# Optimization experiments

Hardware: AMD Instinct MI355X
Metric: run time of the kernel (lower is better)

The kernel has to match this reference:

```python
import jax, jax.numpy as jnp
import numpy as np

B, S, D, H, DK = 4, 1024, 1024, 16, 64  # batch, seq (nq=nk=max_seq_len), d_model, heads, d_kqv
NEG = -1e9
BERN_P = 0.3


def setup_inputs() -> dict:
    key = jax.random.key(0)
    ks = jax.random.split(key, 12)
    xavier = lambda k, fi, fo: jax.random.uniform(k, (fi, fo), minval=-1.0, maxval=1.0) * np.sqrt(6.0 / (fi + fo))
    return {
        "x": jax.random.normal(ks[0], (B, S, D), dtype=jnp.float32),
        "mask": jax.random.randint(ks[1], (B, S), 0, 2).astype(bool),
        "pos_att": jax.random.normal(ks[2], (B, S, S), dtype=jnp.float32),
        "decoder_mask": 1,
        "Wq": xavier(ks[3], D, H * DK), "bq": jnp.zeros((H * DK,), jnp.float32),
        "Wk": xavier(ks[4], D, H * DK), "bk": jnp.zeros((H * DK,), jnp.float32),
        "Wv": xavier(ks[5], D, H * DK), "bv": jnp.zeros((H * DK,), jnp.float32),
        "Wo": xavier(ks[6], H * DK, D), "bo": jnp.zeros((D,), jnp.float32),
    }


def _forward(x, pos_att, Wq, bq, Wk, bk, Wv, bv, Wo, bo, mask, decoder_mask):
    b_s, nq, _ = x.shape
    nk = nq  # self-attention
    relu = jax.nn.relu
    # projections (Linear + activation), split into heads
    q = relu(x @ Wq + bq).reshape(b_s, nq, H, DK).transpose(0, 2, 1, 3)  # [b,h,q,d]
    k = relu(x @ Wk + bk).reshape(b_s, nk, H, DK).transpose(0, 2, 1, 3)  # [b,h,k,d]
    v = relu(x @ Wv + bv).reshape(b_s, nk, H, DK).transpose(0, 2, 1, 3)  # [b,h,k,d]
    att = jnp.einsum("bhqd,bhkd->bhqk", q, k) / np.sqrt(DK).astype(np.float32)
    # positional bias broadcast over heads
    att = att + pos_att[:, None, :, :]
    # bernoulli(0.3) noise: each kept score gets -1e9 added (deterministic key)
    bern = jax.random.bernoulli(jax.random.key(42), BERN_P, att.shape)
    att = att + bern.astype(att.dtype) * NEG
    # key-padding mask [b,1,1,nk]
    att = jnp.where(mask[:, None, None, :], NEG, att)
    # causal triu mask (decoder_mask=True path)
    if decoder_mask:
        tri = jnp.triu(jnp.ones((nq, nk), dtype=bool), k=1)
        att = jnp.where(tri[None, None, :, :], NEG, att)
    att = jax.nn.softmax(att, axis=-1)
    out = jnp.einsum("bhqk,bhkd->bqhd", att, v).reshape(b_s, nq, H * DK)
    out = relu(out @ Wo + bo)
    return out


def reference(x, mask, pos_att, decoder_mask, Wq, bq, Wk, bk, Wv, bv, Wo, bo):
    return _forward(x, pos_att, Wq, bq, Wk, bk, Wv, bv, Wo, bo, mask, decoder_mask)
```

## Files before the change

kernel.cpp:

```cpp
#include <hip/hip_runtime.h>
#include <hip/hip_bf16.h>

#define NEGV (-1e9f)

typedef __attribute__((ext_vector_type(4))) float f32x4;
typedef __attribute__((ext_vector_type(8))) short short8;

#define MFMA_BF16(a, b, c) __builtin_amdgcn_mfma_f32_16x16x32_bf16((a), (b), (c), 0, 0, 0)

#define GLOAD_LDS16(gsrc, ldst)                                                        \
    __builtin_amdgcn_global_load_lds(                                                  \
        (const __attribute__((address_space(1))) unsigned int*)(gsrc),                 \
        (__attribute__((address_space(3))) unsigned int*)(ldst), 16, 0, 0)

#define GLOAD_LDS4(gsrc, ldst)                                                         \
    __builtin_amdgcn_global_load_lds(                                                  \
        (const __attribute__((address_space(1))) unsigned int*)(gsrc),                 \
        (__attribute__((address_space(3))) unsigned int*)(ldst), 4, 0, 0)

__device__ __forceinline__ unsigned short f2bf(float f) {
    union { float f; unsigned u; } v; v.f = f;
    return (unsigned short)((v.u + 0x7fffu + ((v.u >> 16) & 1u)) >> 16);
}

__device__ __forceinline__ float bf2f(unsigned short u) {
    return __uint_as_float((unsigned)u << 16);
}

#define ROTL(x, r) __builtin_amdgcn_alignbit((x), (x), 32 - (r))

__device__ __forceinline__ unsigned tf_bits(unsigned idx) {
    const unsigned ks0 = 0u, ks1 = 42u, ks2 = 0x1BD11BDAu ^ 0u ^ 42u;
    unsigned x0 = ks0, x1 = idx + ks1;
#define TFR(r) { x0 += x1; x1 = ROTL(x1, (r)); x1 ^= x0; }
    TFR(13) TFR(15) TFR(26) TFR(6)   x0 += ks1; x1 += ks2 + 1u;
    TFR(17) TFR(29) TFR(16) TFR(24)  x0 += ks2; x1 += ks0 + 2u;
    TFR(13) TFR(15) TFR(26) TFR(6)   x0 += ks0; x1 += ks1 + 3u;
    TFR(17) TFR(29) TFR(16) TFR(24)  x0 += ks1; x1 += ks2 + 4u;
    TFR(13) TFR(15) TFR(26) TFR(6)   x0 += ks2; x1 += ks0 + 5u;
#undef TFR
    return x0 ^ x1;
}
#define BERN_THRESH 1288490496u

__global__ __launch_bounds__(256) void prep_bern_kernel(
    const float* __restrict__ x,
    const float* __restrict__ Wq, const float* __restrict__ Wk,
    const float* __restrict__ Wv, const float* __restrict__ Wo,
    const float* __restrict__ bq, const float* __restrict__ bk,
    const float* __restrict__ bv,
    const unsigned* __restrict__ mraw, const unsigned* __restrict__ dec,
    unsigned short* __restrict__ xb, unsigned short* __restrict__ wcat,
    unsigned short* __restrict__ wto, float* __restrict__ bcat,
    int* __restrict__ mcanon, unsigned long long* __restrict__ bw) {
    __shared__ float ts[64][68];
    __shared__ int fl_gt1, fl_nf, fl_odz;
    const int bid = blockIdx.x;
    const int t = threadIdx.x;

    if (bid & 1) {
        const int dm = (dec[0] != 0u) ? 1 : 0;
        const int wgid = ((bid >> 1) << 2) + (t >> 6);
        const int lane = t & 63;
        const int G = dm ? 139264 : 262144;
        for (int g = wgid; g < G; g += 6144) {
            int f = __builtin_amdgcn_readfirstlane(g) << 2;
            int kw;
            if (dm) {
                kw = 0;
                while (f >= ((16 - kw) << 12)) { f -= (16 - kw) << 12; ++kw; }
            } else {
                kw = f >> 16; f &= 65535;
            }
            const int qoff = f >> 6;
            const int bh0 = f & 63;
            const int q = (dm ? (kw << 6) : 0) + qoff;
            const unsigned base = ((unsigned)q << 10) + ((unsigned)kw << 6) + (unsigned)lane;
            const unsigned i0 = base + ((unsigned)(bh0 + 0) << 20);
            const unsigned i1 = base + ((unsigned)(bh0 + 1) << 20);
            const unsigned i2 = base + ((unsigned)(bh0 + 2) << 20);
            const unsigned i3 = base + ((unsigned)(bh0 + 3) << 20);
            const unsigned r0 = tf_bits(i0), r1 = tf_bits(i1);
            const unsigned r2 = tf_bits(i2), r3 = tf_bits(i3);
            const unsigned long long w0 = __ballot(r0 < BERN_THRESH);
            const unsigned long long w1 = __ballot(r1 < BERN_THRESH);
            const unsigned long long w2 = __ballot(r2 < BERN_THRESH);
            const unsigned long long w3 = __ballot(r3 < BERN_THRESH);
            if (lane == 0) {
                const size_t rb = ((size_t)(((bh0 << 10) + q) << 4)) + (size_t)kw;
                bw[rb]         = w0;
                bw[rb + 16384] = w1;
                bw[rb + 32768] = w2;
                bw[rb + 49152] = w3;
            }
        }
    } else {
        const int idx = bid >> 1;
        if (idx < 1024) {
            const int which = idx >> 8, tile = idx & 255;
            const float* W = (which == 0) ? Wq : (which == 1) ? Wk : (which == 2) ? Wv : Wo;
            unsigned short* WT = (which < 3) ? (wcat + (size_t)which * 1048576u) : wto;
            const int k0 = (tile >> 4) * 64, n0 = (tile & 15) * 64;
            const int r = t >> 4, c4 = (t & 15) * 4;
#pragma unroll
            for (int rr = 0; rr < 4; ++rr) {
                const int row = r + rr * 16;
                float4 v = *reinterpret_cast<const float4*>(&W[(size_t)(k0 + row) * 1024 + n0 + c4]);
                ts[row][c4 + 0] = v.x; ts[row][c4 + 1] = v.y;
                ts[row][c4 + 2] = v.z; ts[row][c4 + 3] = v.w;
            }
            __syncthreads();
#pragma unroll
            for (int rr = 0; rr < 4; ++rr) {
                const int n = r + rr * 16;
                ushort4 o;
                o.x = f2bf(ts[c4 + 0][n]); o.y = f2bf(ts[c4 + 1][n]);
                o.z = f2bf(ts[c4 + 2][n]); o.w = f2bf(ts[c4 + 3][n]);
                *reinterpret_cast<ushort4*>(&WT[(size_t)(n0 + n) * 1024 + k0 + c4]) = o;
            }
        } else if (idx < 1536) {
            const int c = idx - 1024;
            const float* src = x + (size_t)c * 8192;
            unsigned short* dst = xb + (size_t)c * 8192;
#pragma unroll
            for (int j = 0; j < 8; ++j) {
                const int off = j * 1024 + t * 4;
                float4 v = *reinterpret_cast<const float4*>(src + off);
                ushort4 o;
                o.x = f2bf(v.x); o.y = f2bf(v.y); o.z = f2bf(v.z); o.w = f2bf(v.w);
                *reinterpret_cast<ushort4*>(dst + off) = o;
            }
        } else {
            if (t == 0) { fl_gt1 = 0; fl_nf = 0; fl_odz = 0; }
            __syncthreads();
            for (int i = t; i < 1024; i += 256) {
                unsigned w0 = mraw[i];
                if (w0 > 1u) fl_gt1 = 1;
                if (w0 != 0u && w0 != 1u && w0 != 0x3f800000u) fl_nf = 1;
                if ((i & 1) && w0 != 0u) fl_odz = 1;
            }
            __syncthreads();
            int mode;
            if (!fl_gt1)      mode = fl_odz ? 0 : 3;
            else if (!fl_nf)  mode = 2;
            else              mode = 1;
            for (int i = t; i < 4096; i += 256) {
                int v;
                if (mode == 0)      v = (int)mraw[i];
                else if (mode == 1) v = ((const unsigned char*)mraw)[i] ? 1 : 0;
                else if (mode == 2) v = (mraw[i] != 0u) ? 1 : 0;
                else                v = (mraw[2 * i] != 0u) ? 1 : 0;
                mcanon[i] = v;
            }
            for (int i = t; i < 3072; i += 256)
                bcat[i] = (i < 1024) ? bq[i] : ((i < 2048) ? bk[i - 1024] : bv[i - 2048]);
        }
    }
}

template<int MF, int WMODE>
__global__ __launch_bounds__(256) void gemm_bf16(
    const unsigned short* __restrict__ A, const unsigned short* __restrict__ BT,
    const float* __restrict__ bias, void* __restrict__ Cout,
    int M, int N, int K) {
    __shared__ unsigned short As[MF * 2048];
    __shared__ unsigned short Bs[8192];
    const int t = threadIdx.x;
    const int lane = t & 63, w = t >> 6;
    const int wr = w >> 1, wc = w & 1;
    const int lgrp = lane >> 4, l15 = lane & 15;
    const int m0 = blockIdx.y * (MF * 32), n0 = blockIdx.x * 128;
    const int srow = t >> 3;
    const int scol = ((t & 7) ^ (srow & 7)) << 3;
    const int rdsw = (l15 & 7) << 4;
    f32x4 acc[MF][4] = {};

    for (int k0 = 0; k0 < K; k0 += 64) {
#pragma unroll
        for (int s = 0; s < MF; ++s)
            GLOAD_LDS16(&A[(size_t)(m0 + s * 32 + srow) * K + (k0 + scol)], &As[s * 2048 + t * 8]);
#pragma unroll
        for (int s = 0; s < 4; ++s)
            GLOAD_LDS16(&BT[(size_t)(n0 + s * 32 + srow) * K + (k0 + scol)], &Bs[s * 2048 + t * 8]);
        __syncthreads();
#pragma unroll
        for (int kkh = 0; kkh < 2; ++kkh) {
            const int klb = (kkh * 32 + (lgrp << 3)) * 2;
            short8 af[MF], bf[4];
#pragma unroll
            for (int i = 0; i < MF; ++i)
                af[i] = *(const short8*)((const char*)As + (wr * (MF * 16) + i * 16 + l15) * 128 + (klb ^ rdsw));
#pragma unroll
            for (int i = 0; i < 4; ++i)
                bf[i] = *(const short8*)((const char*)Bs + (wc * 64 + i * 16 + l15) * 128 + (klb ^ rdsw));
            __builtin_amdgcn_s_setprio(1);
#pragma unroll
            for (int mf = 0; mf < MF; ++mf)
#pragma unroll
                for (int nf = 0; nf < 4; ++nf)
                    acc[mf][nf] = MFMA_BF16(af[mf], bf[nf], acc[mf][nf]);
            __builtin_amdgcn_s_setprio(0);
        }
        __syncthreads();
    }
#pragma unroll
    for (int nf = 0; nf < 4; ++nf) {
        const int n = n0 + wc * 64 + nf * 16 + l15;
        const float bv = bias[n];
#pragma unroll
        for (int mf = 0; mf < MF; ++mf) {
#pragma unroll
            for (int r = 0; r < 4; ++r) {
                const int m = m0 + wr * (MF * 16) + mf * 16 + (lgrp << 2) + r;
                float v = fmaxf(acc[mf][nf][r] + bv, 0.f);
                if (WMODE == 0) {
                    ((float*)Cout)[(size_t)m * N + n] = v;
                } else if (WMODE == 1) {
                    ((unsigned short*)Cout)[(size_t)m * N + n] = f2bf(v);
                } else {
                    const int which = n >> 10;
                    ((unsigned short*)Cout)[(size_t)which * 4194304u + (size_t)m * 1024 + (n & 1023)] = f2bf(v);
                }
            }
        }
    }
}

__global__ __launch_bounds__(256) void vsum_part(const unsigned short* __restrict__ Vb,
                                                 float* __restrict__ part) {
    const int c = blockIdx.x, b = blockIdx.y, t = threadIdx.x;
    float a0 = 0, a1 = 0, a2 = 0, a3 = 0;
    const unsigned short* src = &Vb[((size_t)(b * 1024 + c * 64)) * 1024 + t * 4];
    for (int r = 0; r < 64; ++r) {
        ushort4 v = *(const ushort4*)(src + (size_t)r * 1024);
        a0 += bf2f(v.x); a1 += bf2f(v.y); a2 += bf2f(v.z); a3 += bf2f(v.w);
    }
    float4 o = {a0, a1, a2, a3};
    *(float4*)&part[(size_t)(b * 16 + c) * 1024 + t * 4] = o;
}

__global__ __launch_bounds__(256) void vsum_reduce(const float* __restrict__ part,
                                                   float* __restrict__ vmean) {
    const int b = blockIdx.x, t = threadIdx.x;
    float4 s = {0, 0, 0, 0};
    for (int c = 0; c < 16; ++c) {
        float4 v = *(const float4*)&part[(size_t)(b * 16 + c) * 1024 + t * 4];
        s.x += v.x; s.y += v.y; s.z += v.z; s.w += v.w;
    }
    const float sc = 1.0f / 1024.0f;
    float4 o = {s.x * sc, s.y * sc, s.z * sc, s.w * sc};
    *(float4*)&vmean[b * 1024 + t * 4] = o;
}

__global__ __launch_bounds__(256) void attn_kernel(
    const unsigned short* __restrict__ Qb, const unsigned short* __restrict__ Kb,
    const unsigned short* __restrict__ Vb, const float* __restrict__ pos,
    const int* __restrict__ mcanon, const unsigned* __restrict__ dec,
    const unsigned long long* __restrict__ bern, const float* __restrict__ vmean,
    unsigned short* __restrict__ AO) {
    const int gx = blockIdx.x, h = blockIdx.y, b = blockIdx.z;
    const int t = threadIdx.x, lane = t & 63, w = t >> 6;
    const int lgrp = lane >> 4, l15 = lane & 15;

    __shared__ unsigned short Ks[4096];
    __shared__ unsigned short VT[4096];
    __shared__ float pos_s[4096];
    __shared__ int mask_s[64];

    const int dm = (dec[0] != 0u) ? 1 : 0;
    const int qt = (int)((0x765489AB3210CDEFull >> (((gx + 4 * b) & 15) << 2)) & 15);
    const int q0 = qt * 64;
    const int ntiles = dm ? (qt + 1) : 16;
    const int qi = q0 + w * 16 + l15;

    const size_t qg = ((size_t)(b * 1024 + qi)) * 1024 + h * 64 + (lgrp << 3);
    const short8 qb0 = *(const short8*)&Qb[qg];
    const short8 qb1 = *(const short8*)&Qb[qg + 32];
    const unsigned browbase = ((unsigned)((b * 16 + h) * 1024 + qi)) * 16u;

    float m = -3e38f, l = 0.f;
    f32x4 osc[4] = {};
    const int qor = w * 16 + (lgrp << 2);

    for (int kt = 0; kt < ntiles; ++kt) {
        const int kbase = kt * 64;
        {
            const int srow = t >> 3;
            const int scol = ((t & 7) ^ (srow & 7)) << 3;
            GLOAD_LDS16(&Kb[((size_t)(b * 1024 + kbase + srow)) * 1024 + h * 64 + scol],
                        &Ks[t * 8]);
            GLOAD_LDS16(&Kb[((size_t)(b * 1024 + kbase + 32 + srow)) * 1024 + h * 64 + scol],
                        &Ks[2048 + t * 8]);
        }
#pragma unroll
        for (int s = 0; s < 4; ++s) {
            const int row = w * 16 + s * 4 + (lane >> 4);
            const int scol = ((lane & 15) ^ (row & 15)) << 2;
            GLOAD_LDS16(&pos[((size_t)(b * 1024 + q0 + row)) * 1024 + kbase + scol],
                        &pos_s[w * 1024 + s * 256 + lane * 4]);
        }
        if (w == 0) GLOAD_LDS4(&mcanon[b * 1024 + kbase + lane], &mask_s[lane]);
        const unsigned long long bwv = bern[browbase + kt];
        {
            const int p = t >> 3;
            const int dblk = (t & 7) << 3;
            const unsigned short* vs = &Vb[((size_t)(b * 1024 + kbase + 2 * p)) * 1024 + h * 64 + dblk];
            short8 v0 = *(const short8*)vs;
            short8 v1 = *(const short8*)(vs + 1024);
#pragma unroll
            for (int j = 0; j < 8; ++j) {
                const int d = dblk + j;
                const int sw = (d & 7) ^ ((d >> 3) & 7);
                unsigned word = (unsigned)(unsigned short)v0[j] |
                                ((unsigned)(unsigned short)v1[j] << 16);
                *(unsigned*)((char*)VT + d * 128 + ((((2 * p) >> 3) ^ sw) << 4) +
                             (((2 * p) & 7) << 1)) = word;
            }
        }
        __syncthreads();

        f32x4 sacc[4] = {};
        __builtin_amdgcn_s_setprio(1);
#pragma unroll
        for (int kkh = 0; kkh < 2; ++kkh) {
            const int klb = (kkh * 32 + (lgrp << 3)) * 2;
            const short8 qf = kkh ? qb1 : qb0;
#pragma unroll
            for (int f = 0; f < 4; ++f) {
                short8 kf = *(const short8*)((const char*)Ks + (f * 16 + l15) * 128 +
                                             (klb ^ ((l15 & 7) << 4)));
                sacc[f] = MFMA_BF16(kf, qf, sacc[f]);
            }
        }
        __builtin_amdgcn_s_setprio(0);

        float p16[4][4];
        float tmax = -3e38f;
#pragma unroll
        for (int f = 0; f < 4; ++f) {
            const f32x4 posq = *(const f32x4*)&pos_s[(w * 16 + l15) * 64 +
                                                     (((f * 4 + lgrp) ^ l15) << 2)];
            const int4 mq = *(const int4*)&mask_s[f * 16 + (lgrp << 2)];
            const int mqa[4] = {mq.x, mq.y, mq.z, mq.w};
            const unsigned nib = (unsigned)(bwv >> (f * 16 + (lgrp << 2))) & 0xFu;
#pragma unroll
            for (int r = 0; r < 4; ++r) {
                const int ki = kbase + f * 16 + (lgrp << 2) + r;
                float lg = NEGV;
                const bool live = (mqa[r] == 0) && !(dm && (ki > qi));
                if (live) {
                    float sc = fmaf(sacc[f][r], 0.125f, posq[r]);
                    sc += ((nib >> r) & 1u) ? NEGV : 0.f;
                    lg = sc;
                }
                p16[f][r] = lg;
                tmax = fmaxf(tmax, lg);
            }
        }
        tmax = fmaxf(tmax, __shfl_xor(tmax, 16, 64));
        tmax = fmaxf(tmax, __shfl_xor(tmax, 32, 64));
        const float mn = fmaxf(m, tmax);
        const float fac = __expf(m - mn);

        float psum = 0.f;
        unsigned pk[4][2];
#pragma unroll
        for (int f = 0; f < 4; ++f) {
#pragma unroll
            for (int rr = 0; rr < 2; ++rr) {
                float pa = __expf(p16[f][2 * rr] - mn);
                float pb = __expf(p16[f][2 * rr + 1] - mn);
                psum += pa + pb;
                pk[f][rr] = (unsigned)f2bf(pa) | ((unsigned)f2bf(pb) << 16);
            }
        }
        psum += __shfl_xor(psum, 16, 64);
        psum += __shfl_xor(psum, 32, 64);
        l = l * fac + psum;
        m = mn;

#pragma unroll
        for (int r = 0; r < 4; ++r) {
            const float fr = __int_as_float(__builtin_amdgcn_ds_bpermute(
                (((lgrp << 2) + r) << 2), __float_as_int(fac)));
#pragma unroll
            for (int nf = 0; nf < 4; ++nf) osc[nf][r] *= fr;
        }

        {
            const int idx0 = ((((lgrp << 1) & 3) << 4) | l15) << 2;
            const int idx1 = (((((lgrp << 1) + 1) & 3) << 4) | l15) << 2;
            const bool hi = (lgrp >> 1) != 0;
#pragma unroll
            for (int kkh = 0; kkh < 2; ++kkh) {
                union { unsigned u[4]; short8 s; } pa;
#pragma unroll
                for (int s2 = 0; s2 < 4; ++s2) {
                    const int rr = s2 & 1;
                    const int idx = (s2 >> 1) ? idx1 : idx0;
                    const unsigned lo = (unsigned)__builtin_amdgcn_ds_bpermute(idx, (int)pk[kkh * 2][rr]);
                    const unsigned hw = (unsigned)__builtin_amdgcn_ds_bpermute(idx, (int)pk[kkh * 2 + 1][rr]);
                    pa.u[s2] = hi ? hw : lo;
                }
                __builtin_amdgcn_s_setprio(1);
#pragma unroll
                for (int nf = 0; nf < 4; ++nf) {
                    const int d = nf * 16 + l15;
                    const int sw = (d & 7) ^ ((d >> 3) & 7);
                    short8 vf = *(const short8*)((const char*)VT + d * 128 +
                                                 ((((kkh << 2) + lgrp) ^ sw) << 4));
                    osc[nf] = MFMA_BF16(pa.s, vf, osc[nf]);
                }
                __builtin_amdgcn_s_setprio(0);
            }
        }
        __syncthreads();
    }

#pragma unroll
    for (int r = 0; r < 4; ++r) {
        const int src = (((lgrp << 2) + r) << 2);
        const float lr = __int_as_float(__builtin_amdgcn_ds_bpermute(src, __float_as_int(l)));
        const float mr = __int_as_float(__builtin_amdgcn_ds_bpermute(src, __float_as_int(m)));
        const int qo = q0 + qor + r;
        const bool dgen = (mr == NEGV);
        const float inv = 1.0f / lr;
#pragma unroll
        for (int nf = 0; nf < 4; ++nf) {
            const int d = nf * 16 + l15;
            float v = dgen ? vmean[b * 1024 + h * 64 + d] : osc[nf][r] * inv;
            AO[((size_t)(b * 1024 + qo)) * 1024 + h * 64 + d] = f2bf(v);
        }
    }
}

extern "C" void kernel_launch(void* const* d_in, const int* in_sizes, int n_in,
                              void* d_out, int out_size, void* d_ws, size_t ws_size,
                              hipStream_t stream) {
    const float* x       = (const float*)d_in[0];
    const unsigned* mraw = (const unsigned*)d_in[1];
    const float* pos     = (const float*)d_in[2];
    const unsigned* dec  = (const unsigned*)d_in[3];
    const float* Wq = (const float*)d_in[4];  const float* bq = (const float*)d_in[5];
    const float* Wk = (const float*)d_in[6];  const float* bk = (const float*)d_in[7];
    const float* Wv = (const float*)d_in[8];  const float* bv = (const float*)d_in[9];
    const float* Wo = (const float*)d_in[10]; const float* bo = (const float*)d_in[11];
    float* out = (float*)d_out;

    char* ws = (char*)d_ws;
    unsigned short* xb   = (unsigned short*)(ws);
    unsigned short* wcat = (unsigned short*)(ws + (8u << 20));
    unsigned short* wto  = wcat + 3u * 1024 * 1024;
    float* bcat          = (float*)(ws + (16u << 20));
    int* mcanon          = (int*)(ws + (16u << 20) + (64u << 10));
    unsigned short* Qb   = (unsigned short*)(ws + (17u << 20));
    unsigned short* Kb   = Qb + 4u * 1024 * 1024;
    unsigned short* Vb   = Qb + 8u * 1024 * 1024;
    unsigned short* AO   = (unsigned short*)(ws + (41u << 20));
    unsigned long long* bern = (unsigned long long*)(ws + (49u << 20));
    float* part  = (float*)(ws);
    float* vmean = (float*)(ws + (1u << 19));

    prep_bern_kernel<<<3073, 256, 0, stream>>>(x, Wq, Wk, Wv, Wo, bq, bk, bv,
                                               mraw, dec, xb, wcat, wto, bcat,
                                               mcanon, bern);

    gemm_bf16<4, 2><<<dim3(24, 32), 256, 0, stream>>>(xb, wcat, bcat, Qb, 4096, 3072, 1024);

    vsum_part<<<dim3(16, 4), 256, 0, stream>>>(Vb, part);
    vsum_reduce<<<4, 256, 0, stream>>>(part, vmean);

    attn_kernel<<<dim3(16, 16, 4), 256, 0, stream>>>(Qb, Kb, Vb, pos, mcanon, dec, bern, vmean, AO);

    gemm_bf16<2, 0><<<dim3(8, 64), 256, 0, stream>>>(AO, wto, bo, out, 4096, 1024, 1024);
}
```

Baseline: 348.9 us.

## Convert pos_att to bf16 in prep and move bernoulli generation after QKV GEMM

The prep kernel now also converts the fp32 positional bias to bf16, so the attention kernel loads half as many bytes into a smaller LDS tile with a new swizzle. Bernoulli mask generation moves out of prep into a new kernel fused with the V column-sum partials, and its work is re-indexed per (bh, q-group) with a causal-bounded key-window loop. Workspace buffers are reshuffled so AO reuses the start of the workspace. The bf16 positional bias loses precision and adds a conversion pass over a 16 MB tensor, and the bernoulli work now sits on the critical path after the GEMM instead of overlapping with prep.

Measured after the change: 320.0 us. 1.09x faster.

```diff
diff --git a/kernel.cpp b/kernel.cpp
--- a/kernel.cpp
+++ b/kernel.cpp
@@ -43,119 +43,139 @@
 }
 #define BERN_THRESH 1288490496u
 
-__global__ __launch_bounds__(256) void prep_bern_kernel(
+__global__ __launch_bounds__(256) void prep_kernel(
     const float* __restrict__ x,
     const float* __restrict__ Wq, const float* __restrict__ Wk,
     const float* __restrict__ Wv, const float* __restrict__ Wo,
     const float* __restrict__ bq, const float* __restrict__ bk,
     const float* __restrict__ bv,
-    const unsigned* __restrict__ mraw, const unsigned* __restrict__ dec,
+    const unsigned* __restrict__ mraw, const float* __restrict__ pos,
     unsigned short* __restrict__ xb, unsigned short* __restrict__ wcat,
     unsigned short* __restrict__ wto, float* __restrict__ bcat,
-    int* __restrict__ mcanon, unsigned long long* __restrict__ bw) {
+    int* __restrict__ mcanon, unsigned short* __restrict__ pos_bf) {
     __shared__ float ts[64][68];
     __shared__ int fl_gt1, fl_nf, fl_odz;
     const int bid = blockIdx.x;
     const int t = threadIdx.x;
 
-    if (bid & 1) {
+    if (bid < 1024) {
+        const int which = bid >> 8, tile = bid & 255;
+        const float* W = (which == 0) ? Wq : (which == 1) ? Wk : (which == 2) ? Wv : Wo;
+        unsigned short* WT = (which < 3) ? (wcat + (size_t)which * 1048576u) : wto;
+        const int k0 = (tile >> 4) * 64, n0 = (tile & 15) * 64;
+        const int r = t >> 4, c4 = (t & 15) * 4;
+#pragma unroll
+        for (int rr = 0; rr < 4; ++rr) {
+            const int row = r + rr * 16;
+            float4 v = *reinterpret_cast<const float4*>(&W[(size_t)(k0 + row) * 1024 + n0 + c4]);
+            ts[row][c4 + 0] = v.x; ts[row][c4 + 1] = v.y;
+            ts[row][c4 + 2] = v.z; ts[row][c4 + 3] = v.w;
+        }
+        __syncthreads();
+#pragma unroll
+        for (int rr = 0; rr < 4; ++rr) {
+            const int n = r + rr * 16;
+            ushort4 o;
+            o.x = f2bf(ts[c4 + 0][n]); o.y = f2bf(ts[c4 + 1][n]);
+            o.z = f2bf(ts[c4 + 2][n]); o.w = f2bf(ts[c4 + 3][n]);
+            *reinterpret_cast<ushort4*>(&WT[(size_t)(n0 + n) * 1024 + k0 + c4]) = o;
+        }
+    } else if (bid < 2048) {
+        const int c = bid - 1024;
+        const float* src = (c < 512) ? (x + (size_t)c * 8192) : (pos + (size_t)(c - 512) * 8192);
+        unsigned short* dst = (c < 512) ? (xb + (size_t)c * 8192) : (pos_bf + (size_t)(c - 512) * 8192);
+#pragma unroll
+        for (int j = 0; j < 8; ++j) {
+            const int off = j * 1024 + t * 4;
+            float4 v = *reinterpret_cast<const float4*>(src + off);
+            ushort4 o;
+            o.x = f2bf(v.x); o.y = f2bf(v.y); o.z = f2bf(v.z); o.w = f2bf(v.w);
+            *reinterpret_cast<ushort4*>(dst + off) = o;
+        }
+    } else {
+        if (t == 0) { fl_gt1 = 0; fl_nf = 0; fl_odz = 0; }
+        __syncthreads();
+        for (int i = t; i < 1024; i += 256) {
+            unsigned w0 = mraw[i];
+            if (w0 > 1u) fl_gt1 = 1;
+            if (w0 != 0u && w0 != 1u && w0 != 0x3f800000u) fl_nf = 1;
+            if ((i & 1) && w0 != 0u) fl_odz = 1;
+        }
+        __syncthreads();
+        int mode;
+        if (!fl_gt1)      mode = fl_odz ? 0 : 3;
+        else if (!fl_nf)  mode = 2;
+        else              mode = 1;
+        for (int i = t; i < 4096; i += 256) {
+            int v;
+            if (mode == 0)      v = (int)mraw[i];
+            else if (mode == 1) v = ((const unsigned char*)mraw)[i] ? 1 : 0;
+            else if (mode == 2) v = (mraw[i] != 0u) ? 1 : 0;
+            else                v = (mraw[2 * i] != 0u) ? 1 : 0;
+            mcanon[i] = v;
+        }
+        for (int i = t; i < 3072; i += 256)
+            bcat[i] = (i < 1024) ? bq[i] : ((i < 2048) ? bk[i - 1024] : bv[i - 2048]);
+    }
+}
+
+__global__ __launch_bounds__(256) void vsum_bern_kernel(
+    const unsigned short* __restrict__ Vb, float* __restrict__ part,
+    const unsigned* __restrict__ dec, unsigned long long* __restrict__ bw) {
+    const int bid = blockIdx.x, t = threadIdx.x;
+    if (bid < 64) {
+        const int c = bid & 15, b = bid >> 4;
+        float a0 = 0, a1 = 0, a2 = 0, a3 = 0;
+        const unsigned short* src = &Vb[((size_t)(b * 1024 + c * 64)) * 1024 + t * 4];
+        for (int r = 0; r < 64; ++r) {
+            ushort4 v = *(const ushort4*)(src + (size_t)r * 1024);
+            a0 += bf2f(v.x); a1 += bf2f(v.y); a2 += bf2f(v.z); a3 += bf2f(v.w);
+        }
+        float4 o = {a0, a1, a2, a3};
+        *(float4*)&part[(size_t)(b * 16 + c) * 1024 + t * 4] = o;
+    } else {
         const int dm = (dec[0] != 0u) ? 1 : 0;
-        const int wgid = ((bid >> 1) << 2) + (t >> 6);
+        const int wv = ((bid - 64) << 2) + (t >> 6);
         const int lane = t & 63;
-        const int G = dm ? 139264 : 262144;
-        for (int g = wgid; g < G; g += 6144) {
-            int f = __builtin_amdgcn_readfirstlane(g) << 2;
-            int kw;
-            if (dm) {
-                kw = 0;
-                while (f >= ((16 - kw) << 12)) { f -= (16 - kw) << 12; ++kw; }
-            } else {
-                kw = f >> 16; f &= 65535;
-            }
-            const int qoff = f >> 6;
-            const int bh0 = f & 63;
-            const int q = (dm ? (kw << 6) : 0) + qoff;
-            const unsigned base = ((unsigned)q << 10) + ((unsigned)kw << 6) + (unsigned)lane;
-            const unsigned i0 = base + ((unsigned)(bh0 + 0) << 20);
-            const unsigned i1 = base + ((unsigned)(bh0 + 1) << 20);
-            const unsigned i2 = base + ((unsigned)(bh0 + 2) << 20);
-            const unsigned i3 = base + ((unsigned)(bh0 + 3) << 20);
-            const unsigned r0 = tf_bits(i0), r1 = tf_bits(i1);
-            const unsigned r2 = tf_bits(i2), r3 = tf_bits(i3);
-            const unsigned long long w0 = __ballot(r0 < BERN_THRESH);
-            const unsigned long long w1 = __ballot(r1 < BERN_THRESH);
-            const unsigned long long w2 = __ballot(r2 < BERN_THRESH);
-            const unsigned long long w3 = __ballot(r3 < BERN_THRESH);
-            if (lane == 0) {
-                const size_t rb = ((size_t)(((bh0 << 10) + q) << 4)) + (size_t)kw;
-                bw[rb]         = w0;
-                bw[rb + 16384] = w1;
-                bw[rb + 32768] = w2;
-                bw[rb + 49152] = w3;
-            }
-        }
-    } else {
-        const int idx = bid >> 1;
-        if (idx < 1024) {
-            const int which = idx >> 8, tile = idx & 255;
-            const float* W = (which == 0) ? Wq : (which == 1) ? Wk : (which == 2) ? Wv : Wo;
-            unsigned short* WT = (which < 3) ? (wcat + (size_t)which * 1048576u) : wto;
-            const int k0 = (tile >> 4) * 64, n0 = (tile & 15) * 64;
-            const int r = t >> 4, c4 = (t & 15) * 4;
-#pragma unroll
-            for (int rr = 0; rr < 4; ++rr) {
-                const int row = r + rr * 16;
-                float4 v = *reinterpret_cast<const float4*>(&W[(size_t)(k0 + row) * 1024 + n0 + c4]);
-                ts[row][c4 + 0] = v.x; ts[row][c4 + 1] = v.y;
-                ts[row][c4 + 2] = v.z; ts[row][c4 + 3] = v.w;
-            }
-            __syncthreads();
-#pragma unroll
-            for (int rr = 0; rr < 4; ++rr) {
-                const int n = r + rr * 16;
-                ushort4 o;
-                o.x = f2bf(ts[c4 + 0][n]); o.y = f2bf(ts[c4 + 1][n]);
-                o.z = f2bf(ts[c4 + 2][n]); o.w = f2bf(ts[c4 + 3][n]);
-                *reinterpret_cast<ushort4*>(&WT[(size_t)(n0 + n) * 1024 + k0 + c4]) = o;
-            }
-        } else if (idx < 1536) {
-            const int c = idx - 1024;
-            const float* src = x + (size_t)c * 8192;
-            unsigned short* dst = xb + (size_t)c * 8192;
-#pragma unroll
-            for (int j = 0; j < 8; ++j) {
-                const int off = j * 1024 + t * 4;
-                float4 v = *reinterpret_cast<const float4*>(src + off);
-                ushort4 o;
-                o.x = f2bf(v.x); o.y = f2bf(v.y); o.z = f2bf(v.z); o.w = f2bf(v.w);
-                *reinterpret_cast<ushort4*>(dst + off) = o;
-            }
-        } else {
-            if (t == 0) { fl_gt1 = 0; fl_nf = 0; fl_odz = 0; }
-            __syncthreads();
-            for (int i = t; i < 1024; i += 256) {
-                unsigned w0 = mraw[i];
-                if (w0 > 1u) fl_gt1 = 1;
-                if (w0 != 0u && w0 != 1u && w0 != 0x3f800000u) fl_nf = 1;
-                if ((i & 1) && w0 != 0u) fl_odz = 1;
-            }
-            __syncthreads();
-            int mode;
-            if (!fl_gt1)      mode = fl_odz ? 0 : 3;
-            else if (!fl_nf)  mode = 2;
-            else              mode = 1;
-            for (int i = t; i < 4096; i += 256) {
-                int v;
-                if (mode == 0)      v = (int)mraw[i];
-                else if (mode == 1) v = ((const unsigned char*)mraw)[i] ? 1 : 0;
-                else if (mode == 2) v = (mraw[i] != 0u) ? 1 : 0;
-                else                v = (mraw[2 * i] != 0u) ? 1 : 0;
-                mcanon[i] = v;
-            }
-            for (int i = t; i < 3072; i += 256)
-                bcat[i] = (i < 1024) ? bq[i] : ((i < 2048) ? bk[i - 1024] : bv[i - 2048]);
-        }
-    }
+        for (int T = wv; T < 16384; T += 2048) {
+            const int j = T >> 6, bh = T & 63;
+            const int q0 = j << 2;
+            const int nw = dm ? ((q0 >> 6) + 1) : 16;
+            const unsigned rowb = ((unsigned)bh << 10) + (unsigned)q0;
+            const unsigned base = (rowb << 10) + (unsigned)lane;
+            const size_t ob = ((size_t)rowb << 4);
+            for (int kw = 0; kw < nw; ++kw) {
+                const unsigned kb2 = base + ((unsigned)kw << 6);
+                const unsigned r0 = tf_bits(kb2);
+                const unsigned r1 = tf_bits(kb2 + 1024u);
+                const unsigned r2 = tf_bits(kb2 + 2048u);
+                const unsigned r3 = tf_bits(kb2 + 3072u);
+                const unsigned long long w0 = __ballot(r0 < BERN_THRESH);
+                const unsigned long long w1 = __ballot(r1 < BERN_THRESH);
+                const unsigned long long w2 = __ballot(r2 < BERN_THRESH);
+                const unsigned long long w3 = __ballot(r3 < BERN_THRESH);
+                if (lane == 0) {
+                    bw[ob + kw]      = w0;
+                    bw[ob + 16 + kw] = w1;
+                    bw[ob + 32 + kw] = w2;
+                    bw[ob + 48 + kw] = w3;
+                }
+            }
+        }
+    }
+}
+
+__global__ __launch_bounds__(256) void vsum_reduce(const float* __restrict__ part,
+                                                   float* __restrict__ vmean) {
+    const int b = blockIdx.x, t = threadIdx.x;
+    float4 s = {0, 0, 0, 0};
+    for (int c = 0; c < 16; ++c) {
+        float4 v = *(const float4*)&part[(size_t)(b * 16 + c) * 1024 + t * 4];
+        s.x += v.x; s.y += v.y; s.z += v.z; s.w += v.w;
+    }
+    const float sc = 1.0f / 1024.0f;
+    float4 o = {s.x * sc, s.y * sc, s.z * sc, s.w * sc};
+    *(float4*)&vmean[b * 1024 + t * 4] = o;
 }
 
 template<int MF, int WMODE>
@@ -226,35 +246,9 @@
     }
 }
 
-__global__ __launch_bounds__(256) void vsum_part(const unsigned short* __restrict__ Vb,
-                                                 float* __restrict__ part) {
-    const int c = blockIdx.x, b = blockIdx.y, t = threadIdx.x;
-    float a0 = 0, a1 = 0, a2 = 0, a3 = 0;
-    const unsigned short* src = &Vb[((size_t)(b * 1024 + c * 64)) * 1024 + t * 4];
-    for (int r = 0; r < 64; ++r) {
-        ushort4 v = *(const ushort4*)(src + (size_t)r * 1024);
-        a0 += bf2f(v.x); a1 += bf2f(v.y); a2 += bf2f(v.z); a3 += bf2f(v.w);
-    }
-    float4 o = {a0, a1, a2, a3};
-    *(float4*)&part[(size_t)(b * 16 + c) * 1024 + t * 4] = o;
-}
-
-__global__ __launch_bounds__(256) void vsum_reduce(const float* __restrict__ part,
-                                                   float* __restrict__ vmean) {
-    const int b = blockIdx.x, t = threadIdx.x;
-    float4 s = {0, 0, 0, 0};
-    for (int c = 0; c < 16; ++c) {
-        float4 v = *(const float4*)&part[(size_t)(b * 16 + c) * 1024 + t * 4];
-        s.x += v.x; s.y += v.y; s.z += v.z; s.w += v.w;
-    }
-    const float sc = 1.0f / 1024.0f;
-    float4 o = {s.x * sc, s.y * sc, s.z * sc, s.w * sc};
-    *(float4*)&vmean[b * 1024 + t * 4] = o;
-}
-
 __global__ __launch_bounds__(256) void attn_kernel(
     const unsigned short* __restrict__ Qb, const unsigned short* __restrict__ Kb,
-    const unsigned short* __restrict__ Vb, const float* __restrict__ pos,
+    const unsigned short* __restrict__ Vb, const unsigned short* __restrict__ pos_bf,
     const int* __restrict__ mcanon, const unsigned* __restrict__ dec,
     const unsigned long long* __restrict__ bern, const float* __restrict__ vmean,
     unsigned short* __restrict__ AO) {
@@ -264,7 +258,7 @@
 
     __shared__ unsigned short Ks[4096];
     __shared__ unsigned short VT[4096];
-    __shared__ float pos_s[4096];
+    __shared__ unsigned short pos_s[4096];
     __shared__ int mask_s[64];
 
     const int dm = (dec[0] != 0u) ? 1 : 0;
@@ -293,11 +287,11 @@
                         &Ks[2048 + t * 8]);
         }
 #pragma unroll
-        for (int s = 0; s < 4; ++s) {
-            const int row = w * 16 + s * 4 + (lane >> 4);
-            const int scol = ((lane & 15) ^ (row & 15)) << 2;
-            GLOAD_LDS16(&pos[((size_t)(b * 1024 + q0 + row)) * 1024 + kbase + scol],
-                        &pos_s[w * 1024 + s * 256 + lane * 4]);
+        for (int s = 0; s < 2; ++s) {
+            const int row = w * 16 + s * 8 + (lane >> 3);
+            const int gcol = ((lane & 7) ^ (row & 7)) << 3;
+            GLOAD_LDS16(&pos_bf[((size_t)(b * 1024 + q0 + row)) * 1024 + kbase + gcol],
+                        &pos_s[w * 1024 + s * 512 + lane * 8]);
         }
         if (w == 0) GLOAD_LDS4(&mcanon[b * 1024 + kbase + lane], &mask_s[lane]);
         const unsigned long long bwv = bern[browbase + kt];
@@ -334,12 +328,15 @@
         }
         __builtin_amdgcn_s_setprio(0);
 
+        const int prow = w * 16 + l15;
         float p16[4][4];
         float tmax = -3e38f;
 #pragma unroll
         for (int f = 0; f < 4; ++f) {
-            const f32x4 posq = *(const f32x4*)&pos_s[(w * 16 + l15) * 64 +
-                                                     (((f * 4 + lgrp) ^ l15) << 2)];
+            const int gsl = ((f << 1) + (lgrp >> 1)) ^ (prow & 7);
+            const ushort4 pv = *(const ushort4*)((const char*)pos_s + prow * 128 +
+                                                 (gsl << 4) + ((lgrp & 1) << 3));
+            const float pr[4] = {bf2f(pv.x), bf2f(pv.y), bf2f(pv.z), bf2f(pv.w)};
             const int4 mq = *(const int4*)&mask_s[f * 16 + (lgrp << 2)];
             const int mqa[4] = {mq.x, mq.y, mq.z, mq.w};
             const unsigned nib = (unsigned)(bwv >> (f * 16 + (lgrp << 2))) & 0xFu;
@@ -349,7 +346,7 @@
                 float lg = NEGV;
                 const bool live = (mqa[r] == 0) && !(dm && (ki > qi));
                 if (live) {
-                    float sc = fmaf(sacc[f][r], 0.125f, posq[r]);
+                    float sc = fmaf(sacc[f][r], 0.125f, pr[r]);
                     sc += ((nib >> r) & 1u) ? NEGV : 0.f;
                     lg = sc;
                 }
@@ -453,24 +450,26 @@
     unsigned short* wto  = wcat + 3u * 1024 * 1024;
     float* bcat          = (float*)(ws + (16u << 20));
     int* mcanon          = (int*)(ws + (16u << 20) + (64u << 10));
+    float* vmean         = (float*)(ws + (16u << 20) + (128u << 10));
     unsigned short* Qb   = (unsigned short*)(ws + (17u << 20));
     unsigned short* Kb   = Qb + 4u * 1024 * 1024;
     unsigned short* Vb   = Qb + 8u * 1024 * 1024;
-    unsigned short* AO   = (unsigned short*)(ws + (41u << 20));
-    unsigned long long* bern = (unsigned long long*)(ws + (49u << 20));
-    float* part  = (float*)(ws);
-    float* vmean = (float*)(ws + (1u << 19));
-
-    prep_bern_kernel<<<3073, 256, 0, stream>>>(x, Wq, Wk, Wv, Wo, bq, bk, bv,
-                                               mraw, dec, xb, wcat, wto, bcat,
-                                               mcanon, bern);
+    unsigned long long* bern = (unsigned long long*)(ws + (41u << 20));
+    unsigned short* pos_bf   = (unsigned short*)(ws + (49u << 20));
+    float* part          = (float*)(ws);
+    unsigned short* AO   = (unsigned short*)(ws);
+
+    prep_kernel<<<2049, 256, 0, stream>>>(x, Wq, Wk, Wv, Wo, bq, bk, bv,
+                                          mraw, pos, xb, wcat, wto, bcat,
+                                          mcanon, pos_bf);
 
     gemm_bf16<4, 2><<<dim3(24, 32), 256, 0, stream>>>(xb, wcat, bcat, Qb, 4096, 3072, 1024);
 
-    vsum_part<<<dim3(16, 4), 256, 0, stream>>>(Vb, part);
+    vsum_bern_kernel<<<576, 256, 0, stream>>>(Vb, part, dec, bern);
     vsum_reduce<<<4, 256, 0, stream>>>(part, vmean);
 
-    attn_kernel<<<dim3(16, 16, 4), 256, 0, stream>>>(Qb, Kb, Vb, pos, mcanon, dec, bern, vmean, AO);
+    attn_kernel<<<dim3(16, 16, 4), 256, 0, stream>>>(Qb, Kb, Vb, pos_bf, mcanon, dec,
+                                                     bern, vmean, AO);
 
     gemm_bf16<2, 0><<<dim3(8, 64), 256, 0, stream>>>(AO, wto, bo, out, 4096, 1024, 1024);
 }
```
